# Kernel optimization log

Hardware: AMD Instinct MI355X
Metric: run time of the kernel (lower is better)

The kernel has to match this reference:

```python
import jax, jax.numpy as jnp
import numpy as np

D = 1024
H = 16
DH = D // H


def setup_inputs() -> dict:
    key = jax.random.key(0)
    ks = jax.random.split(key, 7)
    s = 0.02
    return {
        "z": jax.random.normal(ks[0], (8, 1024, D), dtype=jnp.float32),
        "ln_w": jnp.ones((D,), dtype=jnp.float32),
        "ln_b": jnp.zeros((D,), dtype=jnp.float32),
        "W_qkv": jax.random.normal(ks[1], (D, 3 * D), dtype=jnp.float32) * s,
        "b_qkv": jnp.zeros((3 * D,), dtype=jnp.float32),
        "W_proj": jax.random.normal(ks[2], (D, D), dtype=jnp.float32) * s,
        "b_proj": jnp.zeros((D,), dtype=jnp.float32),
    }


def reference(z, ln_w, ln_b, W_qkv, b_qkv, W_proj, b_proj):
    b, n, d = z.shape
    # Pre-LN
    mu = jnp.mean(z, axis=-1, keepdims=True)
    var = jnp.var(z, axis=-1, keepdims=True)
    zn = (z - mu) / jnp.sqrt(var + 1e-5) * ln_w + ln_b
    # QKV projection: [b, n, 3, H, DH]
    qkv = (zn @ W_qkv + b_qkv).reshape(b, n, 3, H, DH)
    q = qkv[:, :, 0].transpose(0, 2, 1, 3)  # [b, H, n, DH]
    k = qkv[:, :, 1].transpose(0, 2, 1, 3)
    v = qkv[:, :, 2].transpose(0, 2, 1, 3)
    scale = 1.0 / jnp.sqrt(jnp.asarray(DH, dtype=z.dtype))
    scores = jnp.einsum("bhqd,bhkd->bhqk", q, k) * scale
    attn = jax.nn.softmax(scores, axis=-1)
    msa = jnp.einsum("bhqk,bhkd->bhqd", attn, v)  # [b, H, n, DH]
    msa_cat = msa.transpose(0, 2, 1, 3).reshape(b, n, d)
    out = msa_cat @ W_proj + b_proj
    return z + out
```

## Files before the change

kernel.cpp:

```cpp
#include <hip/hip_runtime.h>
#include <stdint.h>

typedef unsigned short u16;
typedef uint8_t u8;
typedef __bf16 bf16x8 __attribute__((ext_vector_type(8)));
typedef float f32x4 __attribute__((ext_vector_type(4)));
typedef int i32x8 __attribute__((ext_vector_type(8)));

#define D_MODEL 1024
#define NHEADS  16
#define DHEAD   64
#define BATCH   8
#define SEQ     1024
#define MTOT    (BATCH*SEQ)

#define GPTR(p) ((const __attribute__((address_space(1))) void*)(p))
#define LPTR(p) ((__attribute__((address_space(3))) void*)(p))

#if defined(__HIP_DEVICE_COMPILE__)
  #define MFMA_FP8_16x16x128(a, b, c) \
      __builtin_amdgcn_mfma_scale_f32_16x16x128_f8f6f4((a), (b), (c), 0, 0, 0, 127, 0, 127)
  #define CVT_PK_FP8(a, b, old, w) __builtin_amdgcn_cvt_pk_fp8_f32((a), (b), (old), (w))
#else
  #define MFMA_FP8_16x16x128(a, b, c) (c)
  #define CVT_PK_FP8(a, b, old, w) (0)
#endif

__device__ __forceinline__ u16 f2bf(float f) {
    union { float f; uint32_t u; } v; v.f = f;
    uint32_t u = v.u;
    u += 0x7fffu + ((u >> 16) & 1u);
    return (u16)(u >> 16);
}

__device__ __forceinline__ uint32_t pklo(int i1, int i0) {
    return __builtin_amdgcn_perm((uint32_t)i1, (uint32_t)i0, 0x05040100u);
}

__global__ __launch_bounds__(256) void prep_inputs(
    const float* __restrict__ z, const float* __restrict__ w,
    const float* __restrict__ b, uint32_t* __restrict__ znf,
    const float* __restrict__ Wqkv, const float* __restrict__ Wproj,
    u8* __restrict__ outQkv, u8* __restrict__ outProj)
{
    __shared__ float red[8];
    __shared__ u8 tile[32][36];
    const int bid = blockIdx.x;
    const int t = threadIdx.x;
    if (bid < MTOT) {
        const int row = bid;
        const float4 v = reinterpret_cast<const float4*>(z + (size_t)row * D_MODEL)[t];
        float s  = v.x + v.y + v.z + v.w;
        float s2 = v.x*v.x + v.y*v.y + v.z*v.z + v.w*v.w;
        #pragma unroll
        for (int off = 32; off; off >>= 1) {
            s  += __shfl_down(s,  off, 64);
            s2 += __shfl_down(s2, off, 64);
        }
        const int wave = t >> 6, lane = t & 63;
        if (lane == 0) { red[wave] = s; red[wave + 4] = s2; }
        __syncthreads();
        if (t == 0) {
            float ts  = red[0] + red[1] + red[2] + red[3];
            float ts2 = red[4] + red[5] + red[6] + red[7];
            float mu  = ts * (1.0f / D_MODEL);
            float var = ts2 * (1.0f / D_MODEL) - mu * mu;
            red[0] = mu; red[1] = rsqrtf(var + 1e-5f);
        }
        __syncthreads();
        const float mu = red[0], rstd = red[1];
        const float4 wv = reinterpret_cast<const float4*>(w)[t];
        const float4 bv = reinterpret_cast<const float4*>(b)[t];
        const float x0 = (v.x - mu) * rstd * wv.x + bv.x;
        const float x1 = (v.y - mu) * rstd * wv.y + bv.y;
        const float x2 = (v.z - mu) * rstd * wv.z + bv.z;
        const float x3 = (v.w - mu) * rstd * wv.w + bv.w;
        int pk = CVT_PK_FP8(x0, x1, 0, false);
        pk = CVT_PK_FP8(x2, x3, pk, true);
        znf[(size_t)row * (D_MODEL / 4) + t] = (uint32_t)pk;
    } else {
        const int bx = bid - MTOT;
        const int cx = bx & 127;
        const int r0 = (bx >> 7) * 32;
        const float* in; u8* out; int C;
        if (cx < 96) { in = Wqkv;  out = outQkv;  C = 3072; }
        else         { in = Wproj; out = outProj; C = 1024; }
        const int c0 = (cx < 96 ? cx : cx - 96) * 32;
        const int tx = t & 31, ty = t >> 5;
        #pragma unroll
        for (int i = 0; i < 4; ++i) {
            const float f = in[(size_t)(r0 + ty + i*8) * C + c0 + tx];
            tile[ty + i*8][tx] = (u8)(CVT_PK_FP8(f, 0.f, 0, false) & 0xFF);
        }
        __syncthreads();
        #pragma unroll
        for (int i = 0; i < 4; ++i)
            out[(size_t)(c0 + ty + i*8) * D_MODEL + r0 + tx] = tile[tx][ty + i*8];
    }
}

#define QSCALE 23.0831207f

#define GEMM_PRELUDE                                                            \
    const int tid = threadIdx.x;                                                \
    const int wave = tid >> 6, lane = tid & 63;                                 \
    const int lm = lane & 15, g = lane >> 4;                                    \
    const int wm = (wave >> 1) * 64, wn = (wave & 1) * 64;                      \
    const int srow = tid >> 3;                                                  \
    const int sseg = tid & 7;                                                   \
    const int sgcol = (sseg ^ (srow & 7)) * 16;                                 \
    const int xl = lm & 7;                                                      \
    const int ca0 = ((2 * g) ^ xl) * 16;                                        \
    const int ca1 = ((2 * g + 1) ^ xl) * 16;

#define FP8_KLOOP(As_, Bs_, A_, Bt_, n0_, MFMA_STMT)                            \
    f32x4 acc[4][4] = {};                                                       \
    for (int k0 = 0; k0 < D_MODEL; k0 += 128) {                                 \
        _Pragma("unroll")                                                       \
        for (int c = 0; c < 4; ++c) {                                           \
            const int r = srow + c * 32;                                        \
            __builtin_amdgcn_global_load_lds(                                   \
                GPTR(&A_[(size_t)(m0 + r) * D_MODEL + k0 + sgcol]),             \
                LPTR(&As_[r * 128 + sseg * 16]), 16, 0, 0);                     \
            __builtin_amdgcn_global_load_lds(                                   \
                GPTR(&Bt_[(size_t)((n0_) + r) * D_MODEL + k0 + sgcol]),         \
                LPTR(&Bs_[r * 128 + sseg * 16]), 16, 0, 0);                     \
        }                                                                       \
        __syncthreads();                                                        \
        i32x8 af[4], bfr[4];                                                    \
        _Pragma("unroll")                                                       \
        for (int i = 0; i < 4; ++i) {                                           \
            const uint4 alo = *reinterpret_cast<const uint4*>(&As_[(wm + i*16 + lm) * 128 + ca0]); \
            const uint4 ahi = *reinterpret_cast<const uint4*>(&As_[(wm + i*16 + lm) * 128 + ca1]); \
            af[i][0] = alo.x; af[i][1] = alo.y; af[i][2] = alo.z; af[i][3] = alo.w; \
            af[i][4] = ahi.x; af[i][5] = ahi.y; af[i][6] = ahi.z; af[i][7] = ahi.w; \
            const uint4 blo = *reinterpret_cast<const uint4*>(&Bs_[(wn + i*16 + lm) * 128 + ca0]); \
            const uint4 bhi = *reinterpret_cast<const uint4*>(&Bs_[(wn + i*16 + lm) * 128 + ca1]); \
            bfr[i][0] = blo.x; bfr[i][1] = blo.y; bfr[i][2] = blo.z; bfr[i][3] = blo.w; \
            bfr[i][4] = bhi.x; bfr[i][5] = bhi.y; bfr[i][6] = bhi.z; bfr[i][7] = bhi.w; \
        }                                                                       \
        _Pragma("unroll")                                                       \
        for (int i = 0; i < 4; ++i)                                             \
            _Pragma("unroll")                                                   \
            for (int j = 0; j < 4; ++j)                                         \
                MFMA_STMT;                                                      \
        __syncthreads();                                                        \
    }

__global__ __launch_bounds__(256, 2) void gemm_qkv(
    const u8* __restrict__ A, const u8* __restrict__ Bt,
    const float* __restrict__ bias,
    u16* __restrict__ q, u16* __restrict__ k, u16* __restrict__ vT)
{
    __shared__ u8 As[128 * 128];
    __shared__ u8 Bs[128 * 128];
    GEMM_PRELUDE
    const int lin = blockIdx.y * 24 + blockIdx.x;
    const int nl  = (lin & 7) * 192 + (lin >> 3);
    const int bx  = nl % 24;
    const int m0  = (nl / 24) * 128;
    if (bx < 16) {
        const int n0 = bx * 128;
        FP8_KLOOP(As, Bs, A, Bt, n0, acc[i][j] = MFMA_FP8_16x16x128(bfr[j], af[i], acc[i][j]))
        const int colbase = n0 + wn;
        const int sel = colbase >> 10;
        const int h = (colbase & 1023) >> 6;
        u16* dst = (sel == 0) ? q : k;
        const float scl = (sel == 0) ? QSCALE : 1.0f;
        #pragma unroll
        for (int j = 0; j < 4; ++j) {
            const int dh0 = j * 16 + 4 * g;
            const float4 bv4 = *reinterpret_cast<const float4*>(&bias[colbase + dh0]);
            #pragma unroll
            for (int i = 0; i < 4; ++i) {
                const int m = m0 + wm + i * 16 + lm;
                const int b = m >> 10, t = m & 1023;
                ushort4 o;
                o.x = f2bf((acc[i][j][0] + bv4.x) * scl);
                o.y = f2bf((acc[i][j][1] + bv4.y) * scl);
                o.z = f2bf((acc[i][j][2] + bv4.z) * scl);
                o.w = f2bf((acc[i][j][3] + bv4.w) * scl);
                *reinterpret_cast<ushort4*>(
                    &dst[(((size_t)(b * NHEADS + h)) * SEQ + t) * DHEAD + dh0]) = o;
            }
        }
    } else {
        const int n0 = 2048 + (bx - 16) * 128;
        FP8_KLOOP(As, Bs, A, Bt, n0, acc[i][j] = MFMA_FP8_16x16x128(af[i], bfr[j], acc[i][j]))
        const int vcol = (n0 - 2048) + wn;
        const int h = vcol >> 6;
        #pragma unroll
        for (int j = 0; j < 4; ++j) {
            const int dh = ((vcol & 63) + j * 16) + lm;
            const float bv = bias[2048 + vcol + j * 16 + lm];
            #pragma unroll
            for (int i = 0; i < 4; ++i) {
                const int t0 = m0 + wm + i * 16 + 4 * g;
                const int b = t0 >> 10, t = t0 & 1023;
                ushort4 o;
                o.x = f2bf(acc[i][j][0] + bv);
                o.y = f2bf(acc[i][j][1] + bv);
                o.z = f2bf(acc[i][j][2] + bv);
                o.w = f2bf(acc[i][j][3] + bv);
                *reinterpret_cast<ushort4*>(
                    &vT[(((size_t)(b * NHEADS + h)) * DHEAD + dh) * SEQ + t]) = o;
            }
        }
    }
}

__global__ __launch_bounds__(256, 2) void gemm_proj(
    const u8* __restrict__ A, const u8* __restrict__ Bt,
    const float* __restrict__ bias, const float* __restrict__ z,
    float* __restrict__ out)
{
    __shared__ u8 As[128 * 128];
    __shared__ u8 Bs[128 * 128];
    GEMM_PRELUDE
    const int lin = blockIdx.y * 8 + blockIdx.x;
    const int nl  = (lin & 7) * 64 + (lin >> 3);
    const int n0  = (nl & 7) * 128;
    const int m0  = (nl >> 3) * 128;
    FP8_KLOOP(As, Bs, A, Bt, n0, acc[i][j] = MFMA_FP8_16x16x128(bfr[j], af[i], acc[i][j]))
    #pragma unroll
    for (int j = 0; j < 4; ++j) {
        const int col0 = n0 + wn + j * 16 + 4 * g;
        const float4 bv4 = *reinterpret_cast<const float4*>(&bias[col0]);
        #pragma unroll
        for (int i = 0; i < 4; ++i) {
            const int m = m0 + wm + i * 16 + lm;
            const size_t idx = (size_t)m * D_MODEL + col0;
            const float4 zv = *reinterpret_cast<const float4*>(&z[idx]);
            float4 ov;
            ov.x = zv.x + acc[i][j][0] + bv4.x;
            ov.y = zv.y + acc[i][j][1] + bv4.y;
            ov.z = zv.z + acc[i][j][2] + bv4.z;
            ov.w = zv.w + acc[i][j][3] + bv4.w;
            *reinterpret_cast<float4*>(&out[idx]) = ov;
        }
    }
}

#define KLD 68
#define EXP2_MAGIC 12582912.0f

__global__ __launch_bounds__(256, 4) void attn_kernel(
    const u16* __restrict__ Q, const u16* __restrict__ K,
    const u16* __restrict__ Vt, u8* __restrict__ msaf)
{
    __shared__ u16 Ks[64 * KLD];
    __shared__ u16 Vs[64 * KLD];
    const int tid = threadIdx.x, wave = tid >> 6, lane = tid & 63;
    const int lm = lane & 15, g = lane >> 4;
    const int bi = blockIdx.x;
    const int bh = bi & 127;
    const int q0 = (bi >> 7) * 128;
    const int b = bh >> 4, h = bh & 15;
    const size_t headBase = (size_t)bh * SEQ * DHEAD;
    const u16* Qh = Q + headBase;
    const u16* Kh = K + headBase;
    const u16* Vh = Vt + headBase;

    const int srow = tid >> 3, sseg = tid & 7;
    const int aA = 16 * (sseg >> 2) + 4 * (sseg & 3);

    const uint4 onesu = {0x3F803F80u, 0x3F803F80u, 0x3F803F80u, 0x3F803F80u};
    const bf16x8 ONES = __builtin_bit_cast(bf16x8, onesu);
    const f32x4 SMINIT = {16250.0f, 16250.0f, 16250.0f, 16250.0f};

    bf16x8 qf[2][2];
    #pragma unroll
    for (int s = 0; s < 2; ++s) {
        const u16* qrow = Qh + (size_t)(q0 + s * 64 + wave * 16 + lm) * DHEAD;
        qf[s][0] = *reinterpret_cast<const bf16x8*>(qrow + g * 8);
        qf[s][1] = *reinterpret_cast<const bf16x8*>(qrow + 32 + g * 8);
    }

    f32x4 o[2][4] = {};
    f32x4 lacc[2] = {};

    for (int j0 = 0; j0 < SEQ; j0 += 64) {
        #pragma unroll
        for (int s2 = 0; s2 < 2; ++s2) {
            const int row = srow + 32 * s2;
            *reinterpret_cast<uint4*>(&Ks[row * KLD + sseg * 8]) =
                *reinterpret_cast<const uint4*>(&Kh[(size_t)(j0 + row) * DHEAD + sseg * 8]);
            const u16* vrow = Vh + (size_t)row * SEQ + j0;
            const uint2 va = *reinterpret_cast<const uint2*>(vrow + aA);
            const uint2 vb = *reinterpret_cast<const uint2*>(vrow + 32 + aA);
            uint4 wv; wv.x = va.x; wv.y = va.y; wv.z = vb.x; wv.w = vb.y;
            *reinterpret_cast<uint4*>(&Vs[row * KLD + sseg * 8]) = wv;
        }
        __syncthreads();

        bf16x8 kf0[4], kf1[4];
        #pragma unroll
        for (int ni = 0; ni < 4; ++ni) {
            kf0[ni] = *reinterpret_cast<const bf16x8*>(&Ks[(ni*16 + lm) * KLD + g * 8]);
            kf1[ni] = *reinterpret_cast<const bf16x8*>(&Ks[(ni*16 + lm) * KLD + 32 + g * 8]);
        }

        bf16x8 pfr[2][2];
        #pragma unroll
        for (int s = 0; s < 2; ++s) {
            f32x4 st[4];
            __builtin_amdgcn_s_setprio(1);
            #pragma unroll
            for (int ni = 0; ni < 4; ++ni) {
                st[ni] = __builtin_amdgcn_mfma_f32_16x16x32_bf16(kf0[ni], qf[s][0], SMINIT, 0, 0, 0);
                st[ni] = __builtin_amdgcn_mfma_f32_16x16x32_bf16(kf1[ni], qf[s][1], st[ni], 0, 0, 0);
            }
            __builtin_amdgcn_s_setprio(0);
            int ip[4][4];
            #pragma unroll
            for (int ni = 0; ni < 4; ++ni)
                #pragma unroll
                for (int r = 0; r < 4; ++r)
                    ip[ni][r] = __builtin_bit_cast(int, st[ni][r] + EXP2_MAGIC);
            #pragma unroll
            for (int c = 0; c < 2; ++c) {
                uint4 u;
                u.x = pklo(ip[c][1],   ip[c][0]);
                u.y = pklo(ip[c][3],   ip[c][2]);
                u.z = pklo(ip[c+2][1], ip[c+2][0]);
                u.w = pklo(ip[c+2][3], ip[c+2][2]);
                pfr[s][c] = __builtin_bit_cast(bf16x8, u);
            }
            lacc[s] = __builtin_amdgcn_mfma_f32_16x16x32_bf16(ONES, pfr[s][0], lacc[s], 0, 0, 0);
            lacc[s] = __builtin_amdgcn_mfma_f32_16x16x32_bf16(ONES, pfr[s][1], lacc[s], 0, 0, 0);
        }

        __builtin_amdgcn_s_setprio(1);
        #pragma unroll
        for (int mt = 0; mt < 4; ++mt) {
            bf16x8 vf0 = *reinterpret_cast<const bf16x8*>(&Vs[(mt*16 + lm) * KLD + g * 8]);
            bf16x8 vf1 = *reinterpret_cast<const bf16x8*>(&Vs[(mt*16 + lm) * KLD + 32 + g * 8]);
            #pragma unroll
            for (int s = 0; s < 2; ++s) {
                o[s][mt] = __builtin_amdgcn_mfma_f32_16x16x32_bf16(vf0, pfr[s][0], o[s][mt], 0, 0, 0);
                o[s][mt] = __builtin_amdgcn_mfma_f32_16x16x32_bf16(vf1, pfr[s][1], o[s][mt], 0, 0, 0);
            }
        }
        __builtin_amdgcn_s_setprio(0);
        __syncthreads();
    }

    #pragma unroll
    for (int s = 0; s < 2; ++s) {
        const float inv = 1.0f / lacc[s][0];
        const int t = q0 + s * 64 + wave * 16 + lm;
        const size_t base = ((size_t)b * SEQ + t) * D_MODEL + h * DHEAD;
        #pragma unroll
        for (int mt = 0; mt < 4; ++mt) {
            const int d0 = mt * 16 + 4 * g;
            int pk = CVT_PK_FP8(o[s][mt][0] * inv, o[s][mt][1] * inv, 0, false);
            pk = CVT_PK_FP8(o[s][mt][2] * inv, o[s][mt][3] * inv, pk, true);
            *reinterpret_cast<uint32_t*>(&msaf[base + d0]) = (uint32_t)pk;
        }
    }
}

extern "C" void kernel_launch(void* const* d_in, const int* in_sizes, int n_in,
                              void* d_out, int out_size, void* d_ws, size_t ws_size,
                              hipStream_t stream) {
    const float* z      = (const float*)d_in[0];
    const float* ln_w   = (const float*)d_in[1];
    const float* ln_b   = (const float*)d_in[2];
    const float* W_qkv  = (const float*)d_in[3];
    const float* b_qkv  = (const float*)d_in[4];
    const float* W_proj = (const float*)d_in[5];
    const float* b_proj = (const float*)d_in[6];
    float* out = (float*)d_out;

    u8* ws = (u8*)d_ws;
    u8*  znf     = ws;
    u8*  wqkvTf  = znf + (size_t)MTOT * D_MODEL;
    u8*  wprojTf = wqkvTf + (size_t)3 * D_MODEL * D_MODEL;
    u8*  msaf    = wprojTf + (size_t)D_MODEL * D_MODEL;
    u16* q       = (u16*)(msaf + (size_t)MTOT * D_MODEL);
    u16* k       = q + (size_t)MTOT * D_MODEL;
    u16* vT      = k + (size_t)MTOT * D_MODEL;

    prep_inputs<<<MTOT + 4096, 256, 0, stream>>>(
        z, ln_w, ln_b, (uint32_t*)znf, W_qkv, W_proj, wqkvTf, wprojTf);
    gemm_qkv<<<dim3(24, MTOT / 128), 256, 0, stream>>>(znf, wqkvTf, b_qkv, q, k, vT);
    attn_kernel<<<BATCH * NHEADS * (SEQ / 128), 256, 0, stream>>>(q, k, vT, msaf);
    gemm_proj<<<dim3(D_MODEL / 128, MTOT / 128), 256, 0, stream>>>(
        msaf, wprojTf, b_proj, z, out);
}
```

Baseline: 200.8 us.

## Double-buffer K/V tiles in attention with register prefetch of next tile

The attention kernel now holds two LDS buffers for K and V. The next tile is loaded from global memory into registers before the compute on the current tile, then written into the other buffer afterwards. This removes one __syncthreads per iteration and hides global load latency behind the MFMA work. In exchange, LDS use doubles and launch bounds drop from 4 to 2 blocks per CU, which may lower occupancy. The last iteration wraps around and loads tile 0 again for nothing.

```diff
diff --git a/kernel.cpp b/kernel.cpp
--- a/kernel.cpp
+++ b/kernel.cpp
@@ -242,14 +242,15 @@
 }
 
 #define KLD 68
+#define TILE_HALF (64 * KLD)
 #define EXP2_MAGIC 12582912.0f
 
-__global__ __launch_bounds__(256, 4) void attn_kernel(
+__global__ __launch_bounds__(256, 2) void attn_kernel(
     const u16* __restrict__ Q, const u16* __restrict__ K,
     const u16* __restrict__ Vt, u8* __restrict__ msaf)
 {
-    __shared__ u16 Ks[64 * KLD];
-    __shared__ u16 Vs[64 * KLD];
+    __shared__ u16 Ks[2 * TILE_HALF];
+    __shared__ u16 Vs[2 * TILE_HALF];
     const int tid = threadIdx.x, wave = tid >> 6, lane = tid & 63;
     const int lm = lane & 15, g = lane >> 4;
     const int bi = blockIdx.x;
@@ -276,28 +277,44 @@
         qf[s][1] = *reinterpret_cast<const bf16x8*>(qrow + 32 + g * 8);
     }
 
+    uint4 kr[2], vr[2];
+    #define STAGE_LOAD(jj)                                                      \
+        _Pragma("unroll")                                                       \
+        for (int s2 = 0; s2 < 2; ++s2) {                                        \
+            const int row = srow + 32 * s2;                                     \
+            kr[s2] = *reinterpret_cast<const uint4*>(                           \
+                &Kh[(size_t)((jj) + row) * DHEAD + sseg * 8]);                  \
+            const u16* vrow = Vh + (size_t)row * SEQ + (jj);                    \
+            const uint2 va = *reinterpret_cast<const uint2*>(vrow + aA);        \
+            const uint2 vb = *reinterpret_cast<const uint2*>(vrow + 32 + aA);   \
+            vr[s2].x = va.x; vr[s2].y = va.y; vr[s2].z = vb.x; vr[s2].w = vb.y; \
+        }
+    #define STAGE_WRITE(bo_)                                                    \
+        _Pragma("unroll")                                                       \
+        for (int s2 = 0; s2 < 2; ++s2) {                                        \
+            const int row = srow + 32 * s2;                                     \
+            *reinterpret_cast<uint4*>(&Ks[(bo_) + row * KLD + sseg * 8]) = kr[s2]; \
+            *reinterpret_cast<uint4*>(&Vs[(bo_) + row * KLD + sseg * 8]) = vr[s2]; \
+        }
+
     f32x4 o[2][4] = {};
     f32x4 lacc[2] = {};
 
-    for (int j0 = 0; j0 < SEQ; j0 += 64) {
-        #pragma unroll
-        for (int s2 = 0; s2 < 2; ++s2) {
-            const int row = srow + 32 * s2;
-            *reinterpret_cast<uint4*>(&Ks[row * KLD + sseg * 8]) =
-                *reinterpret_cast<const uint4*>(&Kh[(size_t)(j0 + row) * DHEAD + sseg * 8]);
-            const u16* vrow = Vh + (size_t)row * SEQ + j0;
-            const uint2 va = *reinterpret_cast<const uint2*>(vrow + aA);
-            const uint2 vb = *reinterpret_cast<const uint2*>(vrow + 32 + aA);
-            uint4 wv; wv.x = va.x; wv.y = va.y; wv.z = vb.x; wv.w = vb.y;
-            *reinterpret_cast<uint4*>(&Vs[row * KLD + sseg * 8]) = wv;
-        }
+    STAGE_LOAD(0)
+    STAGE_WRITE(0)
+    int cur = 0;
+
+    for (int it = 0; it < SEQ / 64; ++it) {
+        const int jn = ((it + 1) & (SEQ / 64 - 1)) * 64;
+        STAGE_LOAD(jn)
         __syncthreads();
+        const int bo = cur * TILE_HALF;
 
         bf16x8 kf0[4], kf1[4];
         #pragma unroll
         for (int ni = 0; ni < 4; ++ni) {
-            kf0[ni] = *reinterpret_cast<const bf16x8*>(&Ks[(ni*16 + lm) * KLD + g * 8]);
-            kf1[ni] = *reinterpret_cast<const bf16x8*>(&Ks[(ni*16 + lm) * KLD + 32 + g * 8]);
+            kf0[ni] = *reinterpret_cast<const bf16x8*>(&Ks[bo + (ni*16 + lm) * KLD + g * 8]);
+            kf1[ni] = *reinterpret_cast<const bf16x8*>(&Ks[bo + (ni*16 + lm) * KLD + 32 + g * 8]);
         }
 
         bf16x8 pfr[2][2];
@@ -333,8 +350,8 @@
         __builtin_amdgcn_s_setprio(1);
         #pragma unroll
         for (int mt = 0; mt < 4; ++mt) {
-            bf16x8 vf0 = *reinterpret_cast<const bf16x8*>(&Vs[(mt*16 + lm) * KLD + g * 8]);
-            bf16x8 vf1 = *reinterpret_cast<const bf16x8*>(&Vs[(mt*16 + lm) * KLD + 32 + g * 8]);
+            bf16x8 vf0 = *reinterpret_cast<const bf16x8*>(&Vs[bo + (mt*16 + lm) * KLD + g * 8]);
+            bf16x8 vf1 = *reinterpret_cast<const bf16x8*>(&Vs[bo + (mt*16 + lm) * KLD + 32 + g * 8]);
             #pragma unroll
             for (int s = 0; s < 2; ++s) {
                 o[s][mt] = __builtin_amdgcn_mfma_f32_16x16x32_bf16(vf0, pfr[s][0], o[s][mt], 0, 0, 0);
@@ -342,7 +359,9 @@
             }
         }
         __builtin_amdgcn_s_setprio(0);
-        __syncthreads();
+
+        STAGE_WRITE((cur ^ 1) * TILE_HALF)
+        cur ^= 1;
     }
 
     #pragma unroll
```

Result: slower. 230.2 us (+14.6%).
